# Kernel tuning notes

Hardware: AMD Instinct MI355X
Metric: run time of the kernel (lower is better)

Reference implementation:

```python
import jax, jax.numpy as jnp
import numpy as np

B, T, D, H = 2, 2048, 1024, 16
DH = D // H  # 64


def setup_inputs() -> dict:
    key = jax.random.key(0)
    ks = jax.random.split(key, 6)
    s = 1.0 / np.sqrt(D)
    return {
        "x": jax.random.normal(ks[0], (B, T, D), dtype=jnp.float32),
        "Wq": jax.random.normal(ks[1], (D, D), dtype=jnp.float32) * s,
        "Wk": jax.random.normal(ks[2], (D, D), dtype=jnp.float32) * s,
        "Wv": jax.random.normal(ks[3], (D, D), dtype=jnp.float32) * s,
        "Wo": jax.random.normal(ks[4], (D, D), dtype=jnp.float32) * s,
        "bo": jnp.zeros((D,), dtype=jnp.float32),
    }


def reference(x, Wq, Wk, Wv, Wo, bo):
    b, t, _ = x.shape
    # projections (torch Linear: x @ W.T; here W stored as [d_in, d_out])
    q = (x @ Wq).reshape(b, t, H, DH).transpose(0, 2, 1, 3)  # [b,H,t,dh]
    k = (x @ Wk).reshape(b, t, H, DH).transpose(0, 2, 1, 3)
    v = (x @ Wv).reshape(b, t, H, DH).transpose(0, 2, 1, 3)
    scores = jnp.einsum("bhqd,bhkd->bhqk", q, k) / np.sqrt(DH).astype(np.float32)
    causal = jnp.tril(jnp.ones((t, t), dtype=bool))  # True = keep
    scores = jnp.where(causal, scores, -jnp.inf)
    weights = jax.nn.softmax(scores, axis=-1)
    ctx = jnp.einsum("bhqk,bhkd->bhqd", weights, v)
    ctx = ctx.transpose(0, 2, 1, 3).reshape(b, t, D)
    return ctx @ Wo + bo
```

## Files before the change

kernel.cpp:

```cpp
#include <hip/hip_runtime.h>


typedef unsigned short u16;
typedef __attribute__((ext_vector_type(8))) short short8;
typedef __attribute__((ext_vector_type(4))) short short4_t;
typedef __attribute__((ext_vector_type(4))) float f32x4;

#define B_ 2
#define T_ 2048
#define D_ 1024
#define H_ 16
#define DH_ 64
#define M_ (B_ * T_)
#define SCALE_LOG2E 0.18033688011112042f
#define NEG_BIG -3.0e4f

#define SLOT_F 4160
#define SLOTS_PER_BH 72
#define OPART_BYTES ((size_t)32 * SLOTS_PER_BH * SLOT_F * 4)
#define WS_BASE_BYTES ((size_t)24 * 1024 * 1024 * 2)

#define GLOAD16(g, l)                                                     \
  __builtin_amdgcn_global_load_lds(                                       \
      (const __attribute__((address_space(1))) void*)(g),                 \
      (__attribute__((address_space(3))) void*)(l), 16, 0, 0)

__device__ __forceinline__ u16 f2bf(float f) {
  union { float f; unsigned u; } v; v.f = f;
  unsigned r = v.u + 0x7fffu + ((v.u >> 16) & 1u);
  return (u16)(r >> 16);
}
__device__ __forceinline__ u16 f2bf_trunc(float f) {
  union { float f; unsigned u; } v; v.f = f;
  return (u16)(v.u >> 16);
}
__device__ __forceinline__ float exp2_raw(float x) {
  float r;
  asm volatile("v_exp_f32 %0, %1" : "=v"(r) : "v"(x));
  return r;
}

__global__ __launch_bounds__(256) void cvt_x(const float* __restrict__ x,
                                             u16* __restrict__ xb) {
  const int i = (blockIdx.x * 256 + threadIdx.x) * 8;
  float4 a = *(const float4*)(x + i);
  float4 b = *(const float4*)(x + i + 4);
  short8 o;
  o[0] = (short)f2bf(a.x); o[1] = (short)f2bf(a.y);
  o[2] = (short)f2bf(a.z); o[3] = (short)f2bf(a.w);
  o[4] = (short)f2bf(b.x); o[5] = (short)f2bf(b.y);
  o[6] = (short)f2bf(b.z); o[7] = (short)f2bf(b.w);
  *(short8*)(xb + i) = o;
}

__global__ __launch_bounds__(256) void transpose_w(
    const float* __restrict__ w0, const float* __restrict__ w1,
    const float* __restrict__ w2, const float* __restrict__ w3,
    u16* __restrict__ outT) {
  __shared__ u16 Tl[64][72];
  const int z = blockIdx.z;
  const float* src = (z == 0) ? w0 : (z == 1) ? w1 : (z == 2) ? w2 : w3;
  const int r0 = blockIdx.y * 64, c0 = blockIdx.x * 64;
  const int tid = threadIdx.x;
  const int rr = tid >> 2, cc = (tid & 3) * 16;

  const float* p = src + (size_t)(r0 + rr) * D_ + c0 + cc;
  float4 f0 = *(const float4*)p;
  float4 f1 = *(const float4*)(p + 4);
  float4 f2 = *(const float4*)(p + 8);
  float4 f3 = *(const float4*)(p + 12);
  Tl[rr][cc + 0] = f2bf(f0.x); Tl[rr][cc + 1] = f2bf(f0.y);
  Tl[rr][cc + 2] = f2bf(f0.z); Tl[rr][cc + 3] = f2bf(f0.w);
  Tl[rr][cc + 4] = f2bf(f1.x); Tl[rr][cc + 5] = f2bf(f1.y);
  Tl[rr][cc + 6] = f2bf(f1.z); Tl[rr][cc + 7] = f2bf(f1.w);
  Tl[rr][cc + 8] = f2bf(f2.x); Tl[rr][cc + 9] = f2bf(f2.y);
  Tl[rr][cc +10] = f2bf(f2.z); Tl[rr][cc +11] = f2bf(f2.w);
  Tl[rr][cc +12] = f2bf(f3.x); Tl[rr][cc +13] = f2bf(f3.y);
  Tl[rr][cc +14] = f2bf(f3.z); Tl[rr][cc +15] = f2bf(f3.w);
  __syncthreads();

  u16* o = outT + (size_t)z * D_ * D_ + (size_t)(c0 + rr) * D_ + r0 + cc;
  short8 x0, x1;
#pragma unroll
  for (int i = 0; i < 8; i++) x0[i] = (short)Tl[cc + i][rr];
#pragma unroll
  for (int i = 0; i < 8; i++) x1[i] = (short)Tl[cc + 8 + i][rr];
  *(short8*)o = x0;
  *(short8*)(o + 8) = x1;
}

__global__ __launch_bounds__(256) void qkv_gemm(
    const u16* __restrict__ x, const u16* __restrict__ wT,
    u16* __restrict__ qkv) {
  __shared__ u16 As[128][32];
  __shared__ u16 Bs[128][32];

  const int z = blockIdx.z;
  const u16* W = wT + (size_t)z * D_ * D_;
  u16* out = qkv + (size_t)z * M_ * D_;
  const int n0 = blockIdx.x * 128;
  const int m0 = blockIdx.y * 128;
  const int tid = threadIdx.x;
  const int lane = tid & 63, w = tid >> 6;
  const int quad = lane >> 4, l16 = lane & 15;
  const int wr = w >> 1, wc = w & 1;

  f32x4 acc[4][4] = {};
  const int grow = w * 16 + (lane >> 2);
  const int gcol = (lane & 3) * 8;
  u16* lA = (u16*)As + w * 512;
  u16* lB = (u16*)Bs + w * 512;

  for (int k0 = 0; k0 < D_; k0 += 32) {
    const u16* gA = x + (size_t)(m0 + grow) * D_ + k0 + gcol;
    const u16* gB = W + (size_t)(n0 + grow) * D_ + k0 + gcol;
    GLOAD16(gA, lA);
    GLOAD16(gA + (size_t)64 * D_, lA + 2048);
    GLOAD16(gB, lB);
    GLOAD16(gB + (size_t)64 * D_, lB + 2048);
    __syncthreads();

    short8 af[4], bf[4];
#pragma unroll
    for (int i = 0; i < 4; i++)
      af[i] = *(const short8*)&As[wr * 64 + i * 16 + l16][quad * 8];
#pragma unroll
    for (int i = 0; i < 4; i++)
      bf[i] = *(const short8*)&Bs[wc * 64 + i * 16 + l16][quad * 8];
#pragma unroll
    for (int i = 0; i < 4; i++)
#pragma unroll
      for (int j = 0; j < 4; j++)
        acc[i][j] = __builtin_amdgcn_mfma_f32_16x16x32_bf16(af[i], bf[j], acc[i][j], 0, 0, 0);
    __syncthreads();
  }

  const float osc = (z == 0) ? SCALE_LOG2E : 1.0f;
#pragma unroll
  for (int i = 0; i < 4; i++) {
#pragma unroll
    for (int j = 0; j < 4; j++) {
      const int n = n0 + wc * 64 + j * 16 + l16;
      const int h = n >> 6, dh = n & 63;
#pragma unroll
      for (int r = 0; r < 4; r++) {
        const int m = m0 + wr * 64 + i * 16 + quad * 4 + r;
        const int b = m >> 11, t = m & (T_ - 1);
        out[(((size_t)(b * H_ + h)) * T_ + t) * DH_ + dh] = f2bf(acc[i][j][r] * osc);
      }
    }
  }
}

__global__ __launch_bounds__(256) void transpose_v(
    const u16* __restrict__ v, u16* __restrict__ vT) {
  __shared__ u16 Tl[64][72];
  const int t0 = blockIdx.x * 64;
  const int bh = blockIdx.y;
  const int tid = threadIdx.x;
  const int rr = tid >> 2, cc = (tid & 3) * 16;

  const u16* p = v + (size_t)bh * T_ * DH_ + (size_t)(t0 + rr) * DH_ + cc;
  short8 a0 = *(const short8*)p;
  short8 a1 = *(const short8*)(p + 8);
  *(short8*)&Tl[rr][cc] = a0;
  *(short8*)&Tl[rr][cc + 8] = a1;
  __syncthreads();

  u16* o = vT + (size_t)bh * DH_ * T_ + (size_t)rr * T_ + t0 + cc;
  short8 x0, x1;
#pragma unroll
  for (int i = 0; i < 8; i++) x0[i] = (short)Tl[cc + i][rr];
#pragma unroll
  for (int i = 0; i < 8; i++) x1[i] = (short)Tl[cc + 8 + i][rr];
  *(short8*)o = x0;
  *(short8*)(o + 8) = x1;
}

__device__ __forceinline__ int slot_base(int qt) {
  return (qt < 16) ? (qt - 8) * 2
       : (qt < 24) ? 16 + (qt - 16) * 3
                   : 40 + (qt - 24) * 4;
}

__global__ __launch_bounds__(128) void attn_chunk(
    const u16* __restrict__ qg, const u16* __restrict__ kg,
    const u16* __restrict__ vtg, u16* __restrict__ ctx,
    float* __restrict__ Opart) {
  __shared__ u16 Ks[64][72];
  __shared__ u16 Vs[64][72];
  __shared__ u16 Ps[2][2][16][72];

  const int cid = 79 - blockIdx.x;
  int qt, c, nc;
  if (cid < 8)       { qt = cid;                    c = 0;               nc = 1; }
  else if (cid < 24) { qt = 8  + ((cid - 8) >> 1);  c = (cid - 8) & 1;   nc = 2; }
  else if (cid < 48) { qt = 16 + (cid - 24) / 3;    c = (cid - 24) % 3;  nc = 3; }
  else               { qt = 24 + ((cid - 48) >> 2); c = (cid - 48) & 3;  nc = 4; }
  const int nt = qt + 1;
  const int kv_lo = (c * nt / nc) * 64;
  const int kv_hi = ((c + 1) * nt / nc) * 64;
  const int q0 = qt * 64;

  const int bh = blockIdx.y;
  const int tid = threadIdx.x;
  const int w = tid >> 6, lane = tid & 63;
  const int quad = lane >> 4, l16 = lane & 15;
  const size_t baseQK = (size_t)bh * T_ * DH_;
  const size_t baseV  = (size_t)bh * DH_ * T_;

  const int qrowA = q0 + w * 32 + l16;
  const int qrowB = qrowA + 16;
  short8 qfA0 = *(const short8*)(qg + baseQK + (size_t)qrowA * DH_ + quad * 8);
  short8 qfA1 = *(const short8*)(qg + baseQK + (size_t)qrowA * DH_ + 32 + quad * 8);
  short8 qfB0 = *(const short8*)(qg + baseQK + (size_t)qrowB * DH_ + quad * 8);
  short8 qfB1 = *(const short8*)(qg + baseQK + (size_t)qrowB * DH_ + 32 + quad * 8);

  f32x4 oaccA[4] = {}, oaccB[4] = {};
  float liA = 0.f, liB = 0.f;

  const int srow = tid >> 1;
  const int scol = (tid & 1) * 32;

  const u16* kp = kg + baseQK + (size_t)(kv_lo + srow) * DH_ + scol;
  const u16* vp = vtg + baseV + (size_t)srow * T_ + kv_lo + scol;
  short8 kr0 = *(const short8*)kp;
  short8 kr1 = *(const short8*)(kp + 8);
  short8 kr2 = *(const short8*)(kp + 16);
  short8 kr3 = *(const short8*)(kp + 24);
  short8 vr0 = *(const short8*)vp;
  short8 vr1 = *(const short8*)(vp + 8);
  short8 vr2 = *(const short8*)(vp + 16);
  short8 vr3 = *(const short8*)(vp + 24);

  for (int kv0 = kv_lo; kv0 < kv_hi; kv0 += 64) {
    __syncthreads();
    *(short8*)&Ks[srow][scol]      = kr0;
    *(short8*)&Ks[srow][scol + 8]  = kr1;
    *(short8*)&Ks[srow][scol + 16] = kr2;
    *(short8*)&Ks[srow][scol + 24] = kr3;
    *(short8*)&Vs[srow][scol]      = vr0;
    *(short8*)&Vs[srow][scol + 8]  = vr1;
    *(short8*)&Vs[srow][scol + 16] = vr2;
    *(short8*)&Vs[srow][scol + 24] = vr3;
    __syncthreads();

    if (kv0 + 64 < kv_hi) {
      const u16* kn = kg + baseQK + (size_t)(kv0 + 64 + srow) * DH_ + scol;
      const u16* vn = vtg + baseV + (size_t)srow * T_ + kv0 + 64 + scol;
      kr0 = *(const short8*)kn;
      kr1 = *(const short8*)(kn + 8);
      kr2 = *(const short8*)(kn + 16);
      kr3 = *(const short8*)(kn + 24);
      vr0 = *(const short8*)vn;
      vr1 = *(const short8*)(vn + 8);
      vr2 = *(const short8*)(vn + 16);
      vr3 = *(const short8*)(vn + 24);
    }

    short8 kf0[4], kf1[4];
#pragma unroll
    for (int cb = 0; cb < 4; cb++) {
      kf0[cb] = *(const short8*)&Ks[cb * 16 + l16][quad * 8];
      kf1[cb] = *(const short8*)&Ks[cb * 16 + l16][32 + quad * 8];
    }

    f32x4 svA[4], svB[4];
    __builtin_amdgcn_s_setprio(1);
#pragma unroll
    for (int cb = 0; cb < 4; cb++) {
      f32x4 z = {};
      svA[cb] = __builtin_amdgcn_mfma_f32_16x16x32_bf16(kf0[cb], qfA0, z, 0, 0, 0);
      svA[cb] = __builtin_amdgcn_mfma_f32_16x16x32_bf16(kf1[cb], qfA1, svA[cb], 0, 0, 0);
      svB[cb] = __builtin_amdgcn_mfma_f32_16x16x32_bf16(kf0[cb], qfB0, z, 0, 0, 0);
      svB[cb] = __builtin_amdgcn_mfma_f32_16x16x32_bf16(kf1[cb], qfB1, svB[cb], 0, 0, 0);
    }
    __builtin_amdgcn_s_setprio(0);

    float pA[4][4], pB[4][4];
    if (kv0 == q0) {
#pragma unroll
      for (int cb = 0; cb < 4; cb++)
#pragma unroll
        for (int r = 0; r < 4; r++) {
          const int kv = kv0 + cb * 16 + quad * 4 + r;
          pA[cb][r] = exp2_raw((kv <= qrowA) ? svA[cb][r] : NEG_BIG);
          pB[cb][r] = exp2_raw((kv <= qrowB) ? svB[cb][r] : NEG_BIG);
        }
    } else {
#pragma unroll
      for (int cb = 0; cb < 4; cb++)
#pragma unroll
        for (int r = 0; r < 4; r++) {
          pA[cb][r] = exp2_raw(svA[cb][r]);
          pB[cb][r] = exp2_raw(svB[cb][r]);
        }
    }
#pragma unroll
    for (int cb = 0; cb < 4; cb++)
#pragma unroll
      for (int r = 0; r < 4; r++) { liA += pA[cb][r]; liB += pB[cb][r]; }

    short8 vf0[4], vf1[4];
#pragma unroll
    for (int cb = 0; cb < 4; cb++) {
      vf0[cb] = *(const short8*)&Vs[cb * 16 + l16][quad * 8];
      vf1[cb] = *(const short8*)&Vs[cb * 16 + l16][32 + quad * 8];
    }

#pragma unroll
    for (int cb = 0; cb < 4; cb++) {
      short4_t pkA, pkB;
#pragma unroll
      for (int r = 0; r < 4; r++) {
        pkA[r] = (short)f2bf_trunc(pA[cb][r]);
        pkB[r] = (short)f2bf_trunc(pB[cb][r]);
      }
      *(short4_t*)&Ps[w][0][l16][cb * 16 + quad * 4] = pkA;
      *(short4_t*)&Ps[w][1][l16][cb * 16 + quad * 4] = pkB;
    }
    short8 paA0 = *(const short8*)&Ps[w][0][l16][quad * 8];
    short8 paA1 = *(const short8*)&Ps[w][0][l16][32 + quad * 8];
    short8 paB0 = *(const short8*)&Ps[w][1][l16][quad * 8];
    short8 paB1 = *(const short8*)&Ps[w][1][l16][32 + quad * 8];
    __builtin_amdgcn_s_setprio(1);
#pragma unroll
    for (int cb = 0; cb < 4; cb++) {
      oaccA[cb] = __builtin_amdgcn_mfma_f32_16x16x32_bf16(vf0[cb], paA0, oaccA[cb], 0, 0, 0);
      oaccA[cb] = __builtin_amdgcn_mfma_f32_16x16x32_bf16(vf1[cb], paA1, oaccA[cb], 0, 0, 0);
      oaccB[cb] = __builtin_amdgcn_mfma_f32_16x16x32_bf16(vf0[cb], paB0, oaccB[cb], 0, 0, 0);
      oaccB[cb] = __builtin_amdgcn_mfma_f32_16x16x32_bf16(vf1[cb], paB1, oaccB[cb], 0, 0, 0);
    }
    __builtin_amdgcn_s_setprio(0);
  }

  liA += __shfl_xor(liA, 16, 64); liA += __shfl_xor(liA, 32, 64);
  liB += __shfl_xor(liB, 16, 64); liB += __shfl_xor(liB, 32, 64);

  if (nc == 1) {
    const int b = bh >> 4, h = bh & 15;
    const float invA = 1.0f / liA, invB = 1.0f / liB;
    u16* outA = ctx + ((size_t)(b * T_ + qrowA)) * D_ + h * 64 + quad * 4;
    u16* outB = ctx + ((size_t)(b * T_ + qrowB)) * D_ + h * 64 + quad * 4;
#pragma unroll
    for (int cb = 0; cb < 4; cb++) {
      short4_t oA, oB;
#pragma unroll
      for (int r = 0; r < 4; r++) {
        oA[r] = (short)f2bf(oaccA[cb][r] * invA);
        oB[r] = (short)f2bf(oaccB[cb][r] * invB);
      }
      *(short4_t*)(outA + cb * 16) = oA;
      *(short4_t*)(outB + cb * 16) = oB;
    }
  } else {
    float* slot = Opart + ((size_t)bh * SLOTS_PER_BH + slot_base(qt) + c) * SLOT_F;
    float* pA = slot + (size_t)(w * 32 + l16) * 64 + quad * 4;
    float* pB = slot + (size_t)(w * 32 + 16 + l16) * 64 + quad * 4;
#pragma unroll
    for (int cb = 0; cb < 4; cb++) {
      *(f32x4*)(pA + cb * 16) = oaccA[cb];
      *(f32x4*)(pB + cb * 16) = oaccB[cb];
    }
    if (quad == 0) {
      slot[4096 + w * 32 + l16] = liA;
      slot[4096 + w * 32 + 16 + l16] = liB;
    }
  }
}

__global__ __launch_bounds__(256) void attn_combine(
    const float* __restrict__ Opart, u16* __restrict__ ctx) {
  __shared__ float ls[64];
  const int qt = blockIdx.x + 8;
  const int bh = blockIdx.y;
  const int nc = 1 + (qt >> 3);
  const float* slot0 = Opart + ((size_t)bh * SLOTS_PER_BH + slot_base(qt)) * SLOT_F;
  const int tid = threadIdx.x;

  if (tid < 64) {
    float s = 0.f;
    for (int c = 0; c < nc; c++) s += slot0[(size_t)c * SLOT_F + 4096 + tid];
    ls[tid] = 1.0f / s;
  }
  __syncthreads();

  const int q = tid >> 2, d0 = (tid & 3) * 16;
  const float* p = slot0 + (size_t)q * 64 + d0;
  f32x4 a0 = *(const f32x4*)(p);
  f32x4 a1 = *(const f32x4*)(p + 4);
  f32x4 a2 = *(const f32x4*)(p + 8);
  f32x4 a3 = *(const f32x4*)(p + 12);
  for (int c = 1; c < nc; c++) {
    const float* pc = p + (size_t)c * SLOT_F;
    a0 += *(const f32x4*)(pc);
    a1 += *(const f32x4*)(pc + 4);
    a2 += *(const f32x4*)(pc + 8);
    a3 += *(const f32x4*)(pc + 12);
  }
  const float inv = ls[q];
  short8 o0, o1;
#pragma unroll
  for (int i = 0; i < 4; i++) {
    o0[i]     = (short)f2bf(a0[i] * inv);
    o0[i + 4] = (short)f2bf(a1[i] * inv);
    o1[i]     = (short)f2bf(a2[i] * inv);
    o1[i + 4] = (short)f2bf(a3[i] * inv);
  }
  const int b = bh >> 4, h = bh & 15;
  u16* op = ctx + ((size_t)(b * T_ + qt * 64 + q)) * D_ + h * 64 + d0;
  *(short8*)op = o0;
  *(short8*)(op + 8) = o1;
}

__global__ __launch_bounds__(128) void attn_mono(
    const u16* __restrict__ qg, const u16* __restrict__ kg,
    const u16* __restrict__ vtg, u16* __restrict__ ctx) {
  __shared__ u16 Ks[64][72];
  __shared__ u16 Vs[64][72];
  __shared__ u16 Ps[2][2][16][72];

  const int qt = gridDim.x - 1 - blockIdx.x;
  const int bh = blockIdx.y;
  const int tid = threadIdx.x;
  const int w = tid >> 6, lane = tid & 63;
  const int quad = lane >> 4, l16 = lane & 15;
  const int q0 = qt * 64;
  const size_t baseQK = (size_t)bh * T_ * DH_;
  const size_t baseV  = (size_t)bh * DH_ * T_;

  const int qrowA = q0 + w * 32 + l16;
  const int qrowB = qrowA + 16;
  short8 qfA0 = *(const short8*)(qg + baseQK + (size_t)qrowA * DH_ + quad * 8);
  short8 qfA1 = *(const short8*)(qg + baseQK + (size_t)qrowA * DH_ + 32 + quad * 8);
  short8 qfB0 = *(const short8*)(qg + baseQK + (size_t)qrowB * DH_ + quad * 8);
  short8 qfB1 = *(const short8*)(qg + baseQK + (size_t)qrowB * DH_ + 32 + quad * 8);

  f32x4 oaccA[4] = {}, oaccB[4] = {};
  float liA = 0.f, liB = 0.f;

  const int srow = tid >> 1;
  const int scol = (tid & 1) * 32;

  const u16* kp = kg + baseQK + (size_t)srow * DH_ + scol;
  const u16* vp = vtg + baseV + (size_t)srow * T_ + scol;
  short8 kr0 = *(const short8*)kp;
  short8 kr1 = *(const short8*)(kp + 8);
  short8 kr2 = *(const short8*)(kp + 16);
  short8 kr3 = *(const short8*)(kp + 24);
  short8 vr0 = *(const short8*)vp;
  short8 vr1 = *(const short8*)(vp + 8);
  short8 vr2 = *(const short8*)(vp + 16);
  short8 vr3 = *(const short8*)(vp + 24);

  for (int kv0 = 0; kv0 <= q0; kv0 += 64) {
    __syncthreads();
    *(short8*)&Ks[srow][scol]      = kr0;
    *(short8*)&Ks[srow][scol + 8]  = kr1;
    *(short8*)&Ks[srow][scol + 16] = kr2;
    *(short8*)&Ks[srow][scol + 24] = kr3;
    *(short8*)&Vs[srow][scol]      = vr0;
    *(short8*)&Vs[srow][scol + 8]  = vr1;
    *(short8*)&Vs[srow][scol + 16] = vr2;
    *(short8*)&Vs[srow][scol + 24] = vr3;
    __syncthreads();
    if (kv0 < q0) {
      const u16* kn = kg + baseQK + (size_t)(kv0 + 64 + srow) * DH_ + scol;
      const u16* vn = vtg + baseV + (size_t)srow * T_ + kv0 + 64 + scol;
      kr0 = *(const short8*)kn;
      kr1 = *(const short8*)(kn + 8);
      kr2 = *(const short8*)(kn + 16);
      kr3 = *(const short8*)(kn + 24);
      vr0 = *(const short8*)vn;
      vr1 = *(const short8*)(vn + 8);
      vr2 = *(const short8*)(vn + 16);
      vr3 = *(const short8*)(vn + 24);
    }

    short8 kf0[4], kf1[4];
#pragma unroll
    for (int cb = 0; cb < 4; cb++) {
      kf0[cb] = *(const short8*)&Ks[cb * 16 + l16][quad * 8];
      kf1[cb] = *(const short8*)&Ks[cb * 16 + l16][32 + quad * 8];
    }

    f32x4 svA[4], svB[4];
#pragma unroll
    for (int cb = 0; cb < 4; cb++) {
      f32x4 z = {};
      svA[cb] = __builtin_amdgcn_mfma_f32_16x16x32_bf16(kf0[cb], qfA0, z, 0, 0, 0);
      svA[cb] = __builtin_amdgcn_mfma_f32_16x16x32_bf16(kf1[cb], qfA1, svA[cb], 0, 0, 0);
      svB[cb] = __builtin_amdgcn_mfma_f32_16x16x32_bf16(kf0[cb], qfB0, z, 0, 0, 0);
      svB[cb] = __builtin_amdgcn_mfma_f32_16x16x32_bf16(kf1[cb], qfB1, svB[cb], 0, 0, 0);
    }

    float pA[4][4], pB[4][4];
    if (kv0 == q0) {
#pragma unroll
      for (int cb = 0; cb < 4; cb++)
#pragma unroll
        for (int r = 0; r < 4; r++) {
          const int kv = kv0 + cb * 16 + quad * 4 + r;
          pA[cb][r] = exp2_raw((kv <= qrowA) ? svA[cb][r] : NEG_BIG);
          pB[cb][r] = exp2_raw((kv <= qrowB) ? svB[cb][r] : NEG_BIG);
        }
    } else {
#pragma unroll
      for (int cb = 0; cb < 4; cb++)
#pragma unroll
        for (int r = 0; r < 4; r++) {
          pA[cb][r] = exp2_raw(svA[cb][r]);
          pB[cb][r] = exp2_raw(svB[cb][r]);
        }
    }
#pragma unroll
    for (int cb = 0; cb < 4; cb++)
#pragma unroll
      for (int r = 0; r < 4; r++) { liA += pA[cb][r]; liB += pB[cb][r]; }

    short8 vf0[4], vf1[4];
#pragma unroll
    for (int cb = 0; cb < 4; cb++) {
      vf0[cb] = *(const short8*)&Vs[cb * 16 + l16][quad * 8];
      vf1[cb] = *(const short8*)&Vs[cb * 16 + l16][32 + quad * 8];
    }

#pragma unroll
    for (int cb = 0; cb < 4; cb++) {
      short4_t pkA, pkB;
#pragma unroll
      for (int r = 0; r < 4; r++) {
        pkA[r] = (short)f2bf_trunc(pA[cb][r]);
        pkB[r] = (short)f2bf_trunc(pB[cb][r]);
      }
      *(short4_t*)&Ps[w][0][l16][cb * 16 + quad * 4] = pkA;
      *(short4_t*)&Ps[w][1][l16][cb * 16 + quad * 4] = pkB;
    }
    short8 paA0 = *(const short8*)&Ps[w][0][l16][quad * 8];
    short8 paA1 = *(const short8*)&Ps[w][0][l16][32 + quad * 8];
    short8 paB0 = *(const short8*)&Ps[w][1][l16][quad * 8];
    short8 paB1 = *(const short8*)&Ps[w][1][l16][32 + quad * 8];
#pragma unroll
    for (int cb = 0; cb < 4; cb++) {
      oaccA[cb] = __builtin_amdgcn_mfma_f32_16x16x32_bf16(vf0[cb], paA0, oaccA[cb], 0, 0, 0);
      oaccA[cb] = __builtin_amdgcn_mfma_f32_16x16x32_bf16(vf1[cb], paA1, oaccA[cb], 0, 0, 0);
      oaccB[cb] = __builtin_amdgcn_mfma_f32_16x16x32_bf16(vf0[cb], paB0, oaccB[cb], 0, 0, 0);
      oaccB[cb] = __builtin_amdgcn_mfma_f32_16x16x32_bf16(vf1[cb], paB1, oaccB[cb], 0, 0, 0);
    }
  }

  liA += __shfl_xor(liA, 16, 64); liA += __shfl_xor(liA, 32, 64);
  liB += __shfl_xor(liB, 16, 64); liB += __shfl_xor(liB, 32, 64);
  const int b = bh >> 4, h = bh & 15;
  const float invA = 1.0f / liA, invB = 1.0f / liB;
  u16* outA = ctx + ((size_t)(b * T_ + qrowA)) * D_ + h * 64 + quad * 4;
  u16* outB = ctx + ((size_t)(b * T_ + qrowB)) * D_ + h * 64 + quad * 4;
#pragma unroll
  for (int cb = 0; cb < 4; cb++) {
    short4_t oA, oB;
#pragma unroll
    for (int r = 0; r < 4; r++) {
      oA[r] = (short)f2bf(oaccA[cb][r] * invA);
      oB[r] = (short)f2bf(oaccB[cb][r] * invB);
    }
    *(short4_t*)(outA + cb * 16) = oA;
    *(short4_t*)(outB + cb * 16) = oB;
  }
}

__global__ __launch_bounds__(256) void out_gemm(
    const u16* __restrict__ ctx, const u16* __restrict__ woT,
    const float* __restrict__ bo, float* __restrict__ out) {
  __shared__ u16 As[64][32];
  __shared__ u16 Bs[128][32];

  const int n0 = blockIdx.x * 128;
  const int m0 = blockIdx.y * 64;
  const int tid = threadIdx.x;
  const int lane = tid & 63, w = tid >> 6;
  const int quad = lane >> 4, l16 = lane & 15;
  const int wr = w >> 1, wc = w & 1;

  f32x4 acc[2][4] = {};
  const int grow = w * 16 + (lane >> 2);
  const int gcol = (lane & 3) * 8;
  u16* lA = (u16*)As + w * 512;
  u16* lB = (u16*)Bs + w * 512;

  for (int k0 = 0; k0 < D_; k0 += 32) {
    const u16* gA = ctx + (size_t)(m0 + grow) * D_ + k0 + gcol;
    const u16* gB = woT + (size_t)(n0 + grow) * D_ + k0 + gcol;
    GLOAD16(gA, lA);
    GLOAD16(gB, lB);
    GLOAD16(gB + (size_t)64 * D_, lB + 2048);
    __syncthreads();

    short8 af[2], bf[4];
#pragma unroll
    for (int i = 0; i < 2; i++)
      af[i] = *(const short8*)&As[wr * 32 + i * 16 + l16][quad * 8];
#pragma unroll
    for (int i = 0; i < 4; i++)
      bf[i] = *(const short8*)&Bs[wc * 64 + i * 16 + l16][quad * 8];
#pragma unroll
    for (int i = 0; i < 2; i++)
#pragma unroll
      for (int j = 0; j < 4; j++)
        acc[i][j] = __builtin_amdgcn_mfma_f32_16x16x32_bf16(af[i], bf[j], acc[i][j], 0, 0, 0);
    __syncthreads();
  }

#pragma unroll
  for (int i = 0; i < 2; i++) {
#pragma unroll
    for (int j = 0; j < 4; j++) {
      const int n = n0 + wc * 64 + j * 16 + l16;
      const float bias = bo[n];
#pragma unroll
      for (int r = 0; r < 4; r++) {
        const int m = m0 + wr * 32 + i * 16 + quad * 4 + r;
        out[(size_t)m * D_ + n] = acc[i][j][r] + bias;
      }
    }
  }
}

extern "C" void kernel_launch(void* const* d_in, const int* in_sizes, int n_in,
                              void* d_out, int out_size, void* d_ws, size_t ws_size,
                              hipStream_t stream) {
  const float* x  = (const float*)d_in[0];
  const float* Wq = (const float*)d_in[1];
  const float* Wk = (const float*)d_in[2];
  const float* Wv = (const float*)d_in[3];
  const float* Wo = (const float*)d_in[4];
  const float* bo = (const float*)d_in[5];
  float* out = (float*)d_out;

  u16* ws  = (u16*)d_ws;
  u16* xb  = ws;
  u16* wT  = xb + (size_t)M_ * D_;
  u16* qkv = wT + (size_t)4 * D_ * D_;
  u16* ctx = qkv + (size_t)3 * M_ * D_;
  u16* vT  = xb;
  float* Opart = (float*)(ctx + (size_t)M_ * D_);

  cvt_x<<<dim3(M_ * D_ / (256 * 8)), 256, 0, stream>>>(x, xb);
  transpose_w<<<dim3(16, 16, 4), 256, 0, stream>>>(Wq, Wk, Wv, Wo, wT);
  qkv_gemm<<<dim3(D_ / 128, M_ / 128, 3), 256, 0, stream>>>(xb, wT, qkv);
  transpose_v<<<dim3(T_ / 64, B_ * H_), 256, 0, stream>>>(qkv + (size_t)2 * M_ * D_, vT);

  if (ws_size >= WS_BASE_BYTES + OPART_BYTES) {
    attn_chunk<<<dim3(80, B_ * H_), 128, 0, stream>>>(
        qkv, qkv + (size_t)M_ * D_, vT, ctx, Opart);
    attn_combine<<<dim3(24, B_ * H_), 256, 0, stream>>>(Opart, ctx);
  } else {
    attn_mono<<<dim3(T_ / 64, B_ * H_), 128, 0, stream>>>(
        qkv, qkv + (size_t)M_ * D_, vT, ctx);
  }

  out_gemm<<<dim3(D_ / 128, M_ / 64), 256, 0, stream>>>(ctx, wT + (size_t)3 * D_ * D_, bo, out);
}
```

Measured before the change: 195.9 us.

## Fuse prep kernels, write V transposed from QKV GEMM, widen GEMM K-tiles

Merges the x conversion and weight transpose kernels into one launch and drops the separate V transpose kernel: the QKV GEMM epilogue writes V directly in [bh, dh, t] layout. Both the QKV and output GEMMs now stage 64-wide K slices per iteration, halving the number of barrier-synchronised loop trips at the cost of doubled LDS usage. The QKV grid is flattened so z is derived from the N index. This removes two kernel launches and one full read/write pass over V, but the transposed V stores are short 4-element writes strided by T.

```diff
diff --git a/kernel.cpp b/kernel.cpp
--- a/kernel.cpp
+++ b/kernel.cpp
@@ -40,28 +40,33 @@
   return r;
 }
 
-__global__ __launch_bounds__(256) void cvt_x(const float* __restrict__ x,
-                                             u16* __restrict__ xb) {
-  const int i = (blockIdx.x * 256 + threadIdx.x) * 8;
-  float4 a = *(const float4*)(x + i);
-  float4 b = *(const float4*)(x + i + 4);
-  short8 o;
-  o[0] = (short)f2bf(a.x); o[1] = (short)f2bf(a.y);
-  o[2] = (short)f2bf(a.z); o[3] = (short)f2bf(a.w);
-  o[4] = (short)f2bf(b.x); o[5] = (short)f2bf(b.y);
-  o[6] = (short)f2bf(b.z); o[7] = (short)f2bf(b.w);
-  *(short8*)(xb + i) = o;
-}
-
-__global__ __launch_bounds__(256) void transpose_w(
-    const float* __restrict__ w0, const float* __restrict__ w1,
-    const float* __restrict__ w2, const float* __restrict__ w3,
+__global__ __launch_bounds__(256) void prep(
+    const float* __restrict__ x, const float* __restrict__ w0,
+    const float* __restrict__ w1, const float* __restrict__ w2,
+    const float* __restrict__ w3, u16* __restrict__ xb,
     u16* __restrict__ outT) {
   __shared__ u16 Tl[64][72];
-  const int z = blockIdx.z;
+  const int id = blockIdx.x;
+  const int tid = threadIdx.x;
+
+  if (id < 2048) {
+    const int i = (id * 256 + tid) * 8;
+    float4 a = *(const float4*)(x + i);
+    float4 b = *(const float4*)(x + i + 4);
+    short8 o;
+    o[0] = (short)f2bf(a.x); o[1] = (short)f2bf(a.y);
+    o[2] = (short)f2bf(a.z); o[3] = (short)f2bf(a.w);
+    o[4] = (short)f2bf(b.x); o[5] = (short)f2bf(b.y);
+    o[6] = (short)f2bf(b.z); o[7] = (short)f2bf(b.w);
+    *(short8*)(xb + i) = o;
+    return;
+  }
+
+  const int id2 = id - 2048;
+  const int z = id2 >> 8;
+  const int rem = id2 & 255;
+  const int r0 = (rem >> 4) * 64, c0 = (rem & 15) * 64;
   const float* src = (z == 0) ? w0 : (z == 1) ? w1 : (z == 2) ? w2 : w3;
-  const int r0 = blockIdx.y * 64, c0 = blockIdx.x * 64;
-  const int tid = threadIdx.x;
   const int rr = tid >> 2, cc = (tid & 3) * 16;
 
   const float* p = src + (size_t)(r0 + rr) * D_ + c0 + cc;
@@ -92,13 +97,11 @@
 __global__ __launch_bounds__(256) void qkv_gemm(
     const u16* __restrict__ x, const u16* __restrict__ wT,
     u16* __restrict__ qkv) {
-  __shared__ u16 As[128][32];
-  __shared__ u16 Bs[128][32];
-
-  const int z = blockIdx.z;
-  const u16* W = wT + (size_t)z * D_ * D_;
-  u16* out = qkv + (size_t)z * M_ * D_;
+  __shared__ u16 As[128][64];
+  __shared__ u16 Bs[128][64];
+
   const int n0 = blockIdx.x * 128;
+  const int z = n0 >> 10;
   const int m0 = blockIdx.y * 128;
   const int tid = threadIdx.x;
   const int lane = tid & 63, w = tid >> 6;
@@ -106,75 +109,89 @@
   const int wr = w >> 1, wc = w & 1;
 
   f32x4 acc[4][4] = {};
-  const int grow = w * 16 + (lane >> 2);
-  const int gcol = (lane & 3) * 8;
+  const int grow = w * 8 + (lane >> 3);
+  const int gcol = (lane & 7) * 8;
   u16* lA = (u16*)As + w * 512;
   u16* lB = (u16*)Bs + w * 512;
 
-  for (int k0 = 0; k0 < D_; k0 += 32) {
+  for (int k0 = 0; k0 < D_; k0 += 64) {
     const u16* gA = x + (size_t)(m0 + grow) * D_ + k0 + gcol;
-    const u16* gB = W + (size_t)(n0 + grow) * D_ + k0 + gcol;
+    const u16* gB = wT + (size_t)(n0 + grow) * D_ + k0 + gcol;
     GLOAD16(gA, lA);
-    GLOAD16(gA + (size_t)64 * D_, lA + 2048);
+    GLOAD16(gA + (size_t)32 * D_, lA + 2048);
+    GLOAD16(gA + (size_t)64 * D_, lA + 4096);
+    GLOAD16(gA + (size_t)96 * D_, lA + 6144);
     GLOAD16(gB, lB);
-    GLOAD16(gB + (size_t)64 * D_, lB + 2048);
-    __syncthreads();
-
-    short8 af[4], bf[4];
-#pragma unroll
-    for (int i = 0; i < 4; i++)
-      af[i] = *(const short8*)&As[wr * 64 + i * 16 + l16][quad * 8];
-#pragma unroll
-    for (int i = 0; i < 4; i++)
-      bf[i] = *(const short8*)&Bs[wc * 64 + i * 16 + l16][quad * 8];
-#pragma unroll
-    for (int i = 0; i < 4; i++)
-#pragma unroll
-      for (int j = 0; j < 4; j++)
-        acc[i][j] = __builtin_amdgcn_mfma_f32_16x16x32_bf16(af[i], bf[j], acc[i][j], 0, 0, 0);
-    __syncthreads();
-  }
-
-  const float osc = (z == 0) ? SCALE_LOG2E : 1.0f;
-#pragma unroll
-  for (int i = 0; i < 4; i++) {
-#pragma unroll
-    for (int j = 0; j < 4; j++) {
-      const int n = n0 + wc * 64 + j * 16 + l16;
-      const int h = n >> 6, dh = n & 63;
-#pragma unroll
-      for (int r = 0; r < 4; r++) {
-        const int m = m0 + wr * 64 + i * 16 + quad * 4 + r;
-        const int b = m >> 11, t = m & (T_ - 1);
-        out[(((size_t)(b * H_ + h)) * T_ + t) * DH_ + dh] = f2bf(acc[i][j][r] * osc);
+    GLOAD16(gB + (size_t)32 * D_, lB + 2048);
+    GLOAD16(gB + (size_t)64 * D_, lB + 4096);
+    GLOAD16(gB + (size_t)96 * D_, lB + 6144);
+    __syncthreads();
+
+    {
+      short8 af[4], bf[4];
+#pragma unroll
+      for (int i = 0; i < 4; i++)
+        af[i] = *(const short8*)&As[wr * 64 + i * 16 + l16][quad * 8];
+#pragma unroll
+      for (int i = 0; i < 4; i++)
+        bf[i] = *(const short8*)&Bs[wc * 64 + i * 16 + l16][quad * 8];
+#pragma unroll
+      for (int i = 0; i < 4; i++)
+#pragma unroll
+        for (int j = 0; j < 4; j++)
+          acc[i][j] = __builtin_amdgcn_mfma_f32_16x16x32_bf16(af[i], bf[j], acc[i][j], 0, 0, 0);
+    }
+    {
+      short8 af[4], bf[4];
+#pragma unroll
+      for (int i = 0; i < 4; i++)
+        af[i] = *(const short8*)&As[wr * 64 + i * 16 + l16][32 + quad * 8];
+#pragma unroll
+      for (int i = 0; i < 4; i++)
+        bf[i] = *(const short8*)&Bs[wc * 64 + i * 16 + l16][32 + quad * 8];
+#pragma unroll
+      for (int i = 0; i < 4; i++)
+#pragma unroll
+        for (int j = 0; j < 4; j++)
+          acc[i][j] = __builtin_amdgcn_mfma_f32_16x16x32_bf16(af[i], bf[j], acc[i][j], 0, 0, 0);
+    }
+    __syncthreads();
+  }
+
+  if (z < 2) {
+    u16* out = qkv + (size_t)z * M_ * D_;
+    const float osc = (z == 0) ? SCALE_LOG2E : 1.0f;
+#pragma unroll
+    for (int i = 0; i < 4; i++) {
+#pragma unroll
+      for (int j = 0; j < 4; j++) {
+        const int n = n0 + wc * 64 + j * 16 + l16;
+        const int h = (n >> 6) & 15, dh = n & 63;
+#pragma unroll
+        for (int r = 0; r < 4; r++) {
+          const int m = m0 + wr * 64 + i * 16 + quad * 4 + r;
+          const int b = m >> 11, t = m & (T_ - 1);
+          out[(((size_t)(b * H_ + h)) * T_ + t) * DH_ + dh] = f2bf(acc[i][j][r] * osc);
+        }
       }
     }
-  }
-}
-
-__global__ __launch_bounds__(256) void transpose_v(
-    const u16* __restrict__ v, u16* __restrict__ vT) {
-  __shared__ u16 Tl[64][72];
-  const int t0 = blockIdx.x * 64;
-  const int bh = blockIdx.y;
-  const int tid = threadIdx.x;
-  const int rr = tid >> 2, cc = (tid & 3) * 16;
-
-  const u16* p = v + (size_t)bh * T_ * DH_ + (size_t)(t0 + rr) * DH_ + cc;
-  short8 a0 = *(const short8*)p;
-  short8 a1 = *(const short8*)(p + 8);
-  *(short8*)&Tl[rr][cc] = a0;
-  *(short8*)&Tl[rr][cc + 8] = a1;
-  __syncthreads();
-
-  u16* o = vT + (size_t)bh * DH_ * T_ + (size_t)rr * T_ + t0 + cc;
-  short8 x0, x1;
-#pragma unroll
-  for (int i = 0; i < 8; i++) x0[i] = (short)Tl[cc + i][rr];
-#pragma unroll
-  for (int i = 0; i < 8; i++) x1[i] = (short)Tl[cc + 8 + i][rr];
-  *(short8*)o = x0;
-  *(short8*)(o + 8) = x1;
+  } else {
+    u16* vt = qkv + (size_t)2 * M_ * D_;
+#pragma unroll
+    for (int i = 0; i < 4; i++) {
+      const int mm = m0 + wr * 64 + i * 16 + quad * 4;
+      const int b = mm >> 11, t = mm & (T_ - 1);
+#pragma unroll
+      for (int j = 0; j < 4; j++) {
+        const int n = n0 + wc * 64 + j * 16 + l16;
+        const int h = (n >> 6) & 15, dh = n & 63;
+        short4_t pk;
+#pragma unroll
+        for (int r = 0; r < 4; r++) pk[r] = (short)f2bf(acc[i][j][r]);
+        *(short4_t*)(vt + ((size_t)(b * H_ + h) * DH_ + dh) * T_ + t) = pk;
+      }
+    }
+  }
 }
 
 __device__ __forceinline__ int slot_base(int qt) {
@@ -571,8 +588,8 @@
 __global__ __launch_bounds__(256) void out_gemm(
     const u16* __restrict__ ctx, const u16* __restrict__ woT,
     const float* __restrict__ bo, float* __restrict__ out) {
-  __shared__ u16 As[64][32];
-  __shared__ u16 Bs[128][32];
+  __shared__ u16 As[64][64];
+  __shared__ u16 Bs[128][64];
 
   const int n0 = blockIdx.x * 128;
   const int m0 = blockIdx.y * 64;
@@ -582,31 +599,37 @@
   const int wr = w >> 1, wc = w & 1;
 
   f32x4 acc[2][4] = {};
-  const int grow = w * 16 + (lane >> 2);
-  const int gcol = (lane & 3) * 8;
+  const int grow = w * 8 + (lane >> 3);
+  const int gcol = (lane & 7) * 8;
   u16* lA = (u16*)As + w * 512;
   u16* lB = (u16*)Bs + w * 512;
 
-  for (int k0 = 0; k0 < D_; k0 += 32) {
+  for (int k0 = 0; k0 < D_; k0 += 64) {
     const u16* gA = ctx + (size_t)(m0 + grow) * D_ + k0 + gcol;
     const u16* gB = woT + (size_t)(n0 + grow) * D_ + k0 + gcol;
     GLOAD16(gA, lA);
+    GLOAD16(gA + (size_t)32 * D_, lA + 2048);
     GLOAD16(gB, lB);
-    GLOAD16(gB + (size_t)64 * D_, lB + 2048);
-    __syncthreads();
-
-    short8 af[2], bf[4];
-#pragma unroll
-    for (int i = 0; i < 2; i++)
-      af[i] = *(const short8*)&As[wr * 32 + i * 16 + l16][quad * 8];
-#pragma unroll
-    for (int i = 0; i < 4; i++)
-      bf[i] = *(const short8*)&Bs[wc * 64 + i * 16 + l16][quad * 8];
-#pragma unroll
-    for (int i = 0; i < 2; i++)
-#pragma unroll
-      for (int j = 0; j < 4; j++)
-        acc[i][j] = __builtin_amdgcn_mfma_f32_16x16x32_bf16(af[i], bf[j], acc[i][j], 0, 0, 0);
+    GLOAD16(gB + (size_t)32 * D_, lB + 2048);
+    GLOAD16(gB + (size_t)64 * D_, lB + 4096);
+    GLOAD16(gB + (size_t)96 * D_, lB + 6144);
+    __syncthreads();
+
+#pragma unroll
+    for (int kh = 0; kh < 2; kh++) {
+      short8 af[2], bf[4];
+#pragma unroll
+      for (int i = 0; i < 2; i++)
+        af[i] = *(const short8*)&As[wr * 32 + i * 16 + l16][kh * 32 + quad * 8];
+#pragma unroll
+      for (int i = 0; i < 4; i++)
+        bf[i] = *(const short8*)&Bs[wc * 64 + i * 16 + l16][kh * 32 + quad * 8];
+#pragma unroll
+      for (int i = 0; i < 2; i++)
+#pragma unroll
+        for (int j = 0; j < 4; j++)
+          acc[i][j] = __builtin_amdgcn_mfma_f32_16x16x32_bf16(af[i], bf[j], acc[i][j], 0, 0, 0);
+    }
     __syncthreads();
   }
 
@@ -641,13 +664,11 @@
   u16* wT  = xb + (size_t)M_ * D_;
   u16* qkv = wT + (size_t)4 * D_ * D_;
   u16* ctx = qkv + (size_t)3 * M_ * D_;
-  u16* vT  = xb;
+  u16* vT  = qkv + (size_t)2 * M_ * D_;
   float* Opart = (float*)(ctx + (size_t)M_ * D_);
 
-  cvt_x<<<dim3(M_ * D_ / (256 * 8)), 256, 0, stream>>>(x, xb);
-  transpose_w<<<dim3(16, 16, 4), 256, 0, stream>>>(Wq, Wk, Wv, Wo, wT);
-  qkv_gemm<<<dim3(D_ / 128, M_ / 128, 3), 256, 0, stream>>>(xb, wT, qkv);
-  transpose_v<<<dim3(T_ / 64, B_ * H_), 256, 0, stream>>>(qkv + (size_t)2 * M_ * D_, vT);
+  prep<<<dim3(3072), 256, 0, stream>>>(x, Wq, Wk, Wv, Wo, xb, wT);
+  qkv_gemm<<<dim3(24, 32), 256, 0, stream>>>(xb, wT, qkv);
 
   if (ws_size >= WS_BASE_BYTES + OPART_BYTES) {
     attn_chunk<<<dim3(80, B_ * H_), 128, 0, stream>>>(
```

Measured after the change: 208.3 us. 1.06x slower.
